# Kernel tuning notes

Hardware: AMD Instinct MI355X
Metric: run time of the kernel (lower is better)

Reference implementation:

```python
import jax, jax.numpy as jnp
import numpy as np

B, D, H, C = 8192, 384, 256, 6
K_MIN, K_MAX = 4, 16
LN_EPS = 1e-5


def setup_inputs() -> dict:
    key = jax.random.key(0)
    ks = jax.random.split(key, 6)
    s = lambda k, shape: (jax.random.normal(k, shape, jnp.float32) * 0.05)
    return {
        "x": jax.random.normal(ks[0], (B, D), jnp.float32),
        "W_proj": s(ks[1], (D, H)), "b_proj": jnp.zeros((H,), jnp.float32),
        "W_tau": s(ks[2], (D, 1)), "b_tau": jnp.zeros((1,), jnp.float32),
        "W_res": s(ks[3], (H, H)), "b_res": jnp.zeros((H,), jnp.float32),
        "ln_g": jnp.ones((H,), jnp.float32), "ln_b": jnp.zeros((H,), jnp.float32),
        "W_fc": s(ks[4], (H, C)), "b_fc": jnp.zeros((C,), jnp.float32),
    }


def reference(x, W_proj, b_proj, W_tau, b_tau, W_res, b_res, ln_g, ln_b, W_fc, b_fc):
    # adaptive k per sample (torch path casts to int -> non-differentiable)
    tau = jax.nn.sigmoid(x @ W_tau + b_tau)[:, 0]                      # [B]
    k = jax.lax.stop_gradient(
        jnp.clip(jnp.round(K_MAX - (K_MAX - K_MIN) * tau), 1, K_MAX)
    ).astype(jnp.int32)                                                # [B]

    # pairwise squared distances (same nearest-neighbor ordering as cdist)
    sq = jnp.sum(x * x, axis=-1)                                       # [B]
    d2 = sq[:, None] + sq[None, :] - 2.0 * (x @ x.T)                   # [B,B]
    _, idx = jax.lax.top_k(-jax.lax.stop_gradient(d2), K_MAX)          # [B,K_MAX] nearest (incl. self)

    h = jax.nn.relu(x @ W_proj + b_proj)                               # [B,H]

    # ragged top-k mean via fixed K_MAX gather + position mask
    gathered = h[idx]                                                  # [B,K_MAX,H]
    mask = (jnp.arange(K_MAX)[None, :] < k[:, None]).astype(h.dtype)   # [B,K_MAX]
    agg = jnp.einsum('bkh,bk->bh', gathered, mask) / k[:, None].astype(h.dtype)

    r = jax.nn.relu(agg @ W_res + b_res)                               # [B,H]
    z = h + r
    mu = jnp.mean(z, axis=-1, keepdims=True)
    var = jnp.var(z, axis=-1, keepdims=True)
    zn = (z - mu) / jnp.sqrt(var + LN_EPS)
    return (zn * ln_g + ln_b) @ W_fc + b_fc                            # [B,C]
```

## Files before the change

### kernel.cpp

```cpp
#include <hip/hip_runtime.h>
#include <hip/hip_fp16.h>
#include <math.h>

#define NROWS 8192
#define DDIM 384
#define HDIM 256
#define CDIM 6
#define LN_EPS 1e-5f
#define DSTR 138

typedef short bf16x8 __attribute__((ext_vector_type(8)));
typedef float f32x4 __attribute__((ext_vector_type(4)));
typedef unsigned short u16x8 __attribute__((ext_vector_type(8)));
typedef unsigned short u16x4 __attribute__((ext_vector_type(4)));
typedef unsigned short u16x2 __attribute__((ext_vector_type(2)));

__device__ __forceinline__ bool dj_better(float d1, int j1, float d2, int j2) {
    return (d1 < d2) || (d1 == d2 && j1 < j2);
}

__device__ __forceinline__ unsigned int umin_(unsigned int a, unsigned int b) { return a < b ? a : b; }
__device__ __forceinline__ unsigned int umax_(unsigned int a, unsigned int b) { return a > b ? a : b; }

__device__ __forceinline__ unsigned short map16f(float v) {
    union { _Float16 f; unsigned short u; } c;
    c.f = (_Float16)v;
    unsigned short b = c.u;
    return (unsigned short)(b ^ (unsigned short)((((short)b) >> 15) | 0x8000));
}

__device__ __forceinline__ float unmap16(unsigned int m16b) {
    unsigned short fb = (m16b & 0x8000u) ? (unsigned short)(m16b ^ 0x8000u)
                                         : (unsigned short)(~m16b);
    union { unsigned short u; _Float16 f; } cv; cv.u = fb;
    return (float)cv.f;
}

__device__ __forceinline__ unsigned short rne_bf16(float v) {
    unsigned int u = __float_as_uint(v);
    u += 0x7fffu + ((u >> 16) & 1u);
    return (unsigned short)(u >> 16);
}

__device__ __forceinline__ void ins8(
    unsigned int& s0, unsigned int& s1, unsigned int& s2, unsigned int& s3,
    unsigned int& s4, unsigned int& s5, unsigned int& s6, unsigned int& s7,
    unsigned int& m, unsigned int key)
{
    if (key < m) {
        s0 = (s0 == m) ? key : s0;
        s1 = (s1 == m) ? key : s1;
        s2 = (s2 == m) ? key : s2;
        s3 = (s3 == m) ? key : s3;
        s4 = (s4 == m) ? key : s4;
        s5 = (s5 == m) ? key : s5;
        s6 = (s6 == m) ? key : s6;
        s7 = (s7 == m) ? key : s7;
        m = umax_(umax_(umax_(s0, s1), umax_(s2, s3)),
                  umax_(umax_(s4, s5), umax_(s6, s7)));
    }
}

__device__ __forceinline__ unsigned int max8_(
    unsigned int s0, unsigned int s1, unsigned int s2, unsigned int s3,
    unsigned int s4, unsigned int s5, unsigned int s6, unsigned int s7)
{
    return umax_(umax_(umax_(s0, s1), umax_(s2, s3)),
                 umax_(umax_(s4, s5), umax_(s6, s7)));
}

__device__ __forceinline__ void sins8(
    unsigned int& s0, unsigned int& s1, unsigned int& s2, unsigned int& s3,
    unsigned int& s4, unsigned int& s5, unsigned int& s6, unsigned int& s7,
    unsigned int key)
{
    unsigned int t = umin_(s0, key);
    s0 = umax_(t, s1); t = umin_(t, s1);
    s1 = umax_(t, s2); t = umin_(t, s2);
    s2 = umax_(t, s3); t = umin_(t, s3);
    s3 = umax_(t, s4); t = umin_(t, s4);
    s4 = umax_(t, s5); t = umin_(t, s5);
    s5 = umax_(t, s6); t = umin_(t, s6);
    s6 = umax_(t, s7); s7 = umin_(t, s7);
}

#define CE_(a, b) { unsigned int hi_ = umax_(a, b), lo_ = umin_(a, b); a = hi_; b = lo_; }
#define SORT8_DESC(s0, s1, s2, s3, s4, s5, s6, s7) \
    CE_(s0, s1) CE_(s2, s3) CE_(s4, s5) CE_(s6, s7) \
    CE_(s0, s2) CE_(s1, s3) CE_(s4, s6) CE_(s5, s7) \
    CE_(s1, s2) CE_(s5, s6) CE_(s0, s4) CE_(s3, s7) \
    CE_(s1, s5) CE_(s2, s6) \
    CE_(s1, s4) CE_(s3, s6) \
    CE_(s2, s4) CE_(s3, s5) \
    CE_(s3, s4)

__global__ void __launch_bounds__(256) prep_kernel(
    const float* __restrict__ x, const float* __restrict__ W_tau,
    const float* __restrict__ b_tau, unsigned short* __restrict__ xb,
    float* __restrict__ sq, int* __restrict__ kk,
    const float* __restrict__ Wp, unsigned short* __restrict__ wpT,
    const float* __restrict__ Wr, unsigned short* __restrict__ wrT)
{
    int tid = threadIdx.x;
    if (blockIdx.x < NROWS / 4) {
        int wave = tid >> 6, lane = tid & 63;
        int row = blockIdx.x * 4 + wave;
        const float* xr = x + (size_t)row * DDIM;
        unsigned short* xbr = xb + (size_t)row * DDIM;
        float s = 0.f, tp = 0.f;
        #pragma unroll
        for (int q = 0; q < 6; ++q) {
            float v = xr[lane + 64 * q];
            xbr[lane + 64 * q] = rne_bf16(v);
            s = fmaf(v, v, s);
            tp = fmaf(v, W_tau[lane + 64 * q], tp);
        }
        #pragma unroll
        for (int off = 32; off > 0; off >>= 1) {
            s += __shfl_xor(s, off);
            tp += __shfl_xor(tp, off);
        }
        if (lane == 0) {
            sq[row] = s;
            float u = tp + b_tau[0];
            float tau = 1.f / (1.f + expf(-u));
            float kf = rintf(16.f - 12.f * tau);
            int k = (int)kf;
            k = min(16, max(1, k));
            kk[row] = k;
        }
    } else {
        int i = (blockIdx.x - NROWS / 4) * 256 + tid;
        if (i < DDIM * HDIM) {
            int k = i / HDIM, n = i % HDIM;
            wpT[(size_t)n * DDIM + k] = rne_bf16(Wp[i]);
        } else {
            int j = i - DDIM * HDIM;
            if (j < HDIM * HDIM) {
                int k = j / HDIM, n = j % HDIM;
                wrT[(size_t)n * HDIM + k] = rne_bf16(Wr[j]);
            }
        }
    }
}

__global__ void __launch_bounds__(256) mfma_gemm_bias_relu_kernel(
    const unsigned short* __restrict__ A, const unsigned short* __restrict__ WT,
    const float* __restrict__ bias, float* __restrict__ out,
    unsigned short* __restrict__ hb, int K)
{
    __shared__ unsigned short Abuf[128 * 32];
    __shared__ unsigned short Bbuf[128 * 32];

    const int tid = threadIdx.x;
    const int wave = tid >> 6;
    const int rowbase = blockIdx.x * 128;
    const int nbase = blockIdx.y * 128;
    const int lane = tid & 63;
    const int wr = (wave >> 1) * 64;
    const int wc = (wave & 1) * 64;
    const int m16 = lane & 15;
    const int kq = lane >> 4;

    const int er0 = tid >> 2;
    const int er1 = 64 + (tid >> 2);
    const int eko = tid & 3;

    f32x4 acc[4][4];
    #pragma unroll
    for (int a = 0; a < 4; ++a)
        #pragma unroll
        for (int b = 0; b < 4; ++b)
            acc[a][b] = (f32x4){0.f, 0.f, 0.f, 0.f};

    for (int kb = 0; kb < K / 32; ++kb) {
        const int k0 = kb * 32;
        __syncthreads();
        __builtin_amdgcn_global_load_lds(
            (const __attribute__((address_space(1))) void*)(A + (size_t)(rowbase + er0) * K + k0 + eko * 8),
            (__attribute__((address_space(3))) void*)((char*)Abuf + (wave * 64) * 16), 16, 0, 0);
        __builtin_amdgcn_global_load_lds(
            (const __attribute__((address_space(1))) void*)(A + (size_t)(rowbase + er1) * K + k0 + eko * 8),
            (__attribute__((address_space(3))) void*)((char*)Abuf + (256 + wave * 64) * 16), 16, 0, 0);
        __builtin_amdgcn_global_load_lds(
            (const __attribute__((address_space(1))) void*)(WT + (size_t)(nbase + er0) * K + k0 + eko * 8),
            (__attribute__((address_space(3))) void*)((char*)Bbuf + (wave * 64) * 16), 16, 0, 0);
        __builtin_amdgcn_global_load_lds(
            (const __attribute__((address_space(1))) void*)(WT + (size_t)(nbase + er1) * K + k0 + eko * 8),
            (__attribute__((address_space(3))) void*)((char*)Bbuf + (256 + wave * 64) * 16), 16, 0, 0);
        __syncthreads();

        bf16x8 af[4], bfr[4];
        #pragma unroll
        for (int s = 0; s < 4; ++s) {
            af[s]  = *(const bf16x8*)&Abuf[(wr + s * 16 + m16) * 32 + kq * 8];
            bfr[s] = *(const bf16x8*)&Bbuf[(wc + s * 16 + m16) * 32 + kq * 8];
        }
        #pragma unroll
        for (int si = 0; si < 4; ++si)
            #pragma unroll
            for (int sj = 0; sj < 4; ++sj)
                acc[si][sj] = __builtin_amdgcn_mfma_f32_16x16x32_bf16(
                    af[si], bfr[sj], acc[si][sj], 0, 0, 0);
    }

    #pragma unroll
    for (int sj = 0; sj < 4; ++sj) {
        int c = nbase + wc + sj * 16 + m16;
        float bc = bias[c];
        #pragma unroll
        for (int si = 0; si < 4; ++si) {
            int r = rowbase + wr + si * 16 + kq * 4;
            #pragma unroll
            for (int v = 0; v < 4; ++v) {
                float val = fmaxf(acc[si][sj][v] + bc, 0.f);
                out[(size_t)(r + v) * HDIM + c] = val;
                if (hb) hb[(size_t)(r + v) * HDIM + c] = rne_bf16(val);
            }
        }
    }
}

__global__ void __launch_bounds__(256) dist_topk_kernel(
    const unsigned short* __restrict__ xb, const float* __restrict__ sq,
    unsigned int* __restrict__ keys)
{
    __shared__ __align__(16) unsigned short SMEM[128 * DSTR];
    unsigned short* Abuf = SMEM;
    unsigned short* Bbuf = SMEM + 128 * 32;
    unsigned short* Dt   = SMEM;

    int t = blockIdx.x;
    int bi = (int)((sqrtf(8.f * (float)t + 1.f) - 1.f) * 0.5f);
    while ((bi + 1) * (bi + 2) / 2 <= t) ++bi;
    while (bi * (bi + 1) / 2 > t) --bi;
    int bj = t - bi * (bi + 1) / 2;

    const int tid = threadIdx.x;
    const int wave = tid >> 6;
    const int lane = tid & 63;
    const int rowbase = bi * 128;
    const int colbase = bj * 128;
    const int wr = (wave >> 1) * 64;
    const int wc = (wave & 1) * 64;
    const int m16 = lane & 15;
    const int kq = lane >> 4;

    const int er0 = tid >> 2;
    const int er1 = 64 + (tid >> 2);
    const int eko = tid & 3;

    f32x4 acc[4][4];
    #pragma unroll
    for (int a = 0; a < 4; ++a)
        #pragma unroll
        for (int b = 0; b < 4; ++b)
            acc[a][b] = (f32x4){0.f, 0.f, 0.f, 0.f};

    for (int kb = 0; kb < DDIM / 32; ++kb) {
        const int k0 = kb * 32;
        __syncthreads();
        __builtin_amdgcn_global_load_lds(
            (const __attribute__((address_space(1))) void*)(xb + (size_t)(rowbase + er0) * DDIM + k0 + eko * 8),
            (__attribute__((address_space(3))) void*)((char*)Abuf + (wave * 64) * 16), 16, 0, 0);
        __builtin_amdgcn_global_load_lds(
            (const __attribute__((address_space(1))) void*)(xb + (size_t)(rowbase + er1) * DDIM + k0 + eko * 8),
            (__attribute__((address_space(3))) void*)((char*)Abuf + (256 + wave * 64) * 16), 16, 0, 0);
        __builtin_amdgcn_global_load_lds(
            (const __attribute__((address_space(1))) void*)(xb + (size_t)(colbase + er0) * DDIM + k0 + eko * 8),
            (__attribute__((address_space(3))) void*)((char*)Bbuf + (wave * 64) * 16), 16, 0, 0);
        __builtin_amdgcn_global_load_lds(
            (const __attribute__((address_space(1))) void*)(xb + (size_t)(colbase + er1) * DDIM + k0 + eko * 8),
            (__attribute__((address_space(3))) void*)((char*)Bbuf + (256 + wave * 64) * 16), 16, 0, 0);
        __syncthreads();

        bf16x8 af[4], bfr[4];
        #pragma unroll
        for (int s = 0; s < 4; ++s) {
            af[s]  = *(const bf16x8*)&Abuf[(wr + s * 16 + m16) * 32 + kq * 8];
            bfr[s] = *(const bf16x8*)&Bbuf[(wc + s * 16 + m16) * 32 + kq * 8];
        }
        #pragma unroll
        for (int si = 0; si < 4; ++si)
            #pragma unroll
            for (int sj = 0; sj < 4; ++sj)
                acc[si][sj] = __builtin_amdgcn_mfma_f32_16x16x32_bf16(
                    af[si], bfr[sj], acc[si][sj], 0, 0, 0);
    }
    __syncthreads();

    const int sr = tid >> 1;
    const int seg = tid & 1;

    {
        float sqc[4];
        #pragma unroll
        for (int sj = 0; sj < 4; ++sj) sqc[sj] = sq[colbase + wc + sj * 16 + m16];
        #pragma unroll
        for (int si = 0; si < 4; ++si)
            #pragma unroll
            for (int sj = 0; sj < 4; ++sj) {
                int r = wr + si * 16 + kq * 4;
                int c = wc + sj * 16 + m16;
                #pragma unroll
                for (int v = 0; v < 4; ++v)
                    Dt[(r + v) * DSTR + c] = map16f(sqc[sj] - 2.0f * acc[si][sj][v]);
            }
        __syncthreads();

        const unsigned short* rowp = &Dt[sr * DSTR + seg * 64];
        const int cb0 = colbase + seg * 64;
        u16x8 c0 = *(const u16x8*)rowp;
        unsigned int s0 = ((unsigned int)c0[0] << 13) | (unsigned int)(cb0 + 0);
        unsigned int s1 = ((unsigned int)c0[1] << 13) | (unsigned int)(cb0 + 1);
        unsigned int s2 = ((unsigned int)c0[2] << 13) | (unsigned int)(cb0 + 2);
        unsigned int s3 = ((unsigned int)c0[3] << 13) | (unsigned int)(cb0 + 3);
        unsigned int s4 = ((unsigned int)c0[4] << 13) | (unsigned int)(cb0 + 4);
        unsigned int s5 = ((unsigned int)c0[5] << 13) | (unsigned int)(cb0 + 5);
        unsigned int s6 = ((unsigned int)c0[6] << 13) | (unsigned int)(cb0 + 6);
        unsigned int s7 = ((unsigned int)c0[7] << 13) | (unsigned int)(cb0 + 7);
        SORT8_DESC(s0, s1, s2, s3, s4, s5, s6, s7);
        #pragma unroll
        for (int i = 1; i < 8; ++i) {
            u16x8 ch = *(const u16x8*)(rowp + i * 8);
            int cb = cb0 + i * 8;
            #pragma unroll
            for (int e = 0; e < 8; ++e)
                sins8(s0, s1, s2, s3, s4, s5, s6, s7,
                      ((unsigned int)ch[e] << 13) | (unsigned int)(cb + e));
        }
        size_t kb = (size_t)(rowbase + sr) * 1024 + (size_t)bj * 16 + seg * 8;
        uint4 o0; o0.x = s0; o0.y = s1; o0.z = s2; o0.w = s3;
        uint4 o1; o1.x = s4; o1.y = s5; o1.z = s6; o1.w = s7;
        *(uint4*)&keys[kb] = o0;
        *(uint4*)&keys[kb + 4] = o1;
    }

    if (bi != bj) {
        __syncthreads();
        #pragma unroll
        for (int si = 0; si < 4; ++si) {
            float4 sqr4 = *(const float4*)&sq[rowbase + wr + si * 16 + kq * 4];
            float srw[4] = {sqr4.x, sqr4.y, sqr4.z, sqr4.w};
            #pragma unroll
            for (int sj = 0; sj < 4; ++sj) {
                int r = wr + si * 16 + kq * 4;
                int c = wc + sj * 16 + m16;
                unsigned short h4[4];
                #pragma unroll
                for (int v = 0; v < 4; ++v)
                    h4[v] = map16f(srw[v] - 2.0f * acc[si][sj][v]);
                *(unsigned long long*)&Dt[c * DSTR + r] = *(unsigned long long*)h4;
            }
        }
        __syncthreads();

        const unsigned short* rowp = &Dt[sr * DSTR + seg * 64];
        const int cb0 = rowbase + seg * 64;
        u16x8 c0 = *(const u16x8*)rowp;
        unsigned int s0 = ((unsigned int)c0[0] << 13) | (unsigned int)(cb0 + 0);
        unsigned int s1 = ((unsigned int)c0[1] << 13) | (unsigned int)(cb0 + 1);
        unsigned int s2 = ((unsigned int)c0[2] << 13) | (unsigned int)(cb0 + 2);
        unsigned int s3 = ((unsigned int)c0[3] << 13) | (unsigned int)(cb0 + 3);
        unsigned int s4 = ((unsigned int)c0[4] << 13) | (unsigned int)(cb0 + 4);
        unsigned int s5 = ((unsigned int)c0[5] << 13) | (unsigned int)(cb0 + 5);
        unsigned int s6 = ((unsigned int)c0[6] << 13) | (unsigned int)(cb0 + 6);
        unsigned int s7 = ((unsigned int)c0[7] << 13) | (unsigned int)(cb0 + 7);
        SORT8_DESC(s0, s1, s2, s3, s4, s5, s6, s7);
        #pragma unroll
        for (int i = 1; i < 8; ++i) {
            u16x8 ch = *(const u16x8*)(rowp + i * 8);
            int cb = cb0 + i * 8;
            #pragma unroll
            for (int e = 0; e < 8; ++e)
                sins8(s0, s1, s2, s3, s4, s5, s6, s7,
                      ((unsigned int)ch[e] << 13) | (unsigned int)(cb + e));
        }
        size_t kb = (size_t)(colbase + sr) * 1024 + (size_t)bi * 16 + seg * 8;
        uint4 o0; o0.x = s0; o0.y = s1; o0.z = s2; o0.w = s3;
        uint4 o1; o1.x = s4; o1.y = s5; o1.z = s6; o1.w = s7;
        *(uint4*)&keys[kb] = o0;
        *(uint4*)&keys[kb + 4] = o1;
    }
}

__global__ void __launch_bounds__(256) topk_rescore_agg_kernel(
    const unsigned int* __restrict__ keys, const float* __restrict__ x,
    const float* __restrict__ sq, const int* __restrict__ kk,
    const unsigned short* __restrict__ hb, unsigned short* __restrict__ aggb)
{
    const int w = threadIdx.x >> 6;
    const int row = blockIdx.x * 4 + w;
    const int lane = threadIdx.x & 63;
    __shared__ int sidx[4][16];

    const uint4* kp = (const uint4*)(keys + (size_t)row * 1024 + lane * 16);
    uint4 v0 = kp[0], v1 = kp[1];
    unsigned int s0 = v0.x, s1 = v0.y, s2 = v0.z, s3 = v0.w;
    unsigned int s4 = v1.x, s5 = v1.y, s6 = v1.z, s7 = v1.w;
    unsigned int m = max8_(s0, s1, s2, s3, s4, s5, s6, s7);
    #pragma unroll
    for (int q = 2; q < 4; ++q) {
        uint4 v = kp[q];
        unsigned int gmin = umin_(umin_(v.x, v.y), umin_(v.z, v.w));
        if (gmin < m) {
            ins8(s0, s1, s2, s3, s4, s5, s6, s7, m, v.x);
            ins8(s0, s1, s2, s3, s4, s5, s6, s7, m, v.y);
            ins8(s0, s1, s2, s3, s4, s5, s6, s7, m, v.z);
            ins8(s0, s1, s2, s3, s4, s5, s6, s7, m, v.w);
        }
    }
    unsigned int lmin = umin_(umin_(umin_(s0, s1), umin_(s2, s3)),
                              umin_(umin_(s4, s5), umin_(s6, s7)));
    unsigned int myout = 0;
    for (int t = 0; t < 32; ++t) {
        unsigned int wv = lmin;
        #pragma unroll
        for (int off = 32; off > 0; off >>= 1)
            wv = umin_(wv, (unsigned int)__shfl_xor((int)wv, off));
        if (lane == t) myout = wv;
        if (lmin == wv) {
            s0 = (s0 == wv) ? 0xFFFFFFFFu : s0;
            s1 = (s1 == wv) ? 0xFFFFFFFFu : s1;
            s2 = (s2 == wv) ? 0xFFFFFFFFu : s2;
            s3 = (s3 == wv) ? 0xFFFFFFFFu : s3;
            s4 = (s4 == wv) ? 0xFFFFFFFFu : s4;
            s5 = (s5 == wv) ? 0xFFFFFFFFu : s5;
            s6 = (s6 == wv) ? 0xFFFFFFFFu : s6;
            s7 = (s7 == wv) ? 0xFFFFFFFFu : s7;
            lmin = umin_(umin_(umin_(s0, s1), umin_(s2, s3)),
                         umin_(umin_(s4, s5), umin_(s6, s7)));
        }
    }
    int myj = (int)(myout & 8191u);
    float dscr = (lane < 32) ? unmap16(myout >> 13) : INFINITY;

    const float EPS2 = 2.5f;
    const int k = kk[row];
    float d_k   = __shfl(dscr, k);
    float d_km1 = __shfl(dscr, k - 1);
    bool cin = false, amb = false;
    if (lane < 32) {
        if (lane < k) { cin = (dscr + EPS2 <= d_k); amb = !cin; }
        else          { amb = (dscr < d_km1 + EPS2); }
    }
    unsigned long long cinmask = __ballot(cin);
    unsigned long long ambmask = __ballot(amb);
    int n_in = __popcll(cinmask);
    int msel = k - n_in;

    float d_ex = 0.f;
    if (msel > 0) {
        float xr[6];
        #pragma unroll
        for (int q = 0; q < 6; ++q) xr[q] = x[(size_t)row * DDIM + lane + 64 * q];
        float sqrow = sq[row];
        unsigned long long mm = ambmask;
        while (mm) {
            int c = (int)(__ffsll(mm) - 1);
            mm &= mm - 1;
            int j = __shfl(myj, c);
            const float* xc = x + (size_t)j * DDIM;
            float p = 0.f;
            #pragma unroll
            for (int q = 0; q < 6; ++q) p = fmaf(xr[q], xc[lane + 64 * q], p);
            #pragma unroll
            for (int off = 32; off > 0; off >>= 1) p += __shfl_xor(p, off);
            float d = sqrow + sq[j] - 2.f * p;
            if (lane == c) d_ex = d;
        }
        int selrank = 0;
        unsigned long long mm2 = ambmask;
        while (mm2) {
            int u = (int)(__ffsll(mm2) - 1);
            mm2 &= mm2 - 1;
            float du = __shfl(d_ex, u);
            int ju = __shfl(myj, u);
            if (u != lane && dj_better(du, ju, d_ex, myj)) ++selrank;
        }
        if (amb && selrank < msel)
            sidx[w][n_in + selrank] = myj;
    }
    if (cin) {
        int pos = __popcll(cinmask & ((1ull << lane) - 1ull));
        sidx[w][pos] = myj;
    }
    __syncthreads();

    float a0 = 0.f, a1 = 0.f, a2 = 0.f, a3 = 0.f;
    for (int t = 0; t < k; ++t) {
        uint2 v = *(const uint2*)(hb + (size_t)sidx[w][t] * HDIM + lane * 4);
        a0 += __uint_as_float(v.x << 16);
        a1 += __uint_as_float(v.x & 0xFFFF0000u);
        a2 += __uint_as_float(v.y << 16);
        a3 += __uint_as_float(v.y & 0xFFFF0000u);
    }
    float inv = 1.f / (float)k;
    unsigned int b0 = rne_bf16(a0 * inv);
    unsigned int b1 = rne_bf16(a1 * inv);
    unsigned int b2 = rne_bf16(a2 * inv);
    unsigned int b3 = rne_bf16(a3 * inv);
    uint2 o; o.x = b0 | (b1 << 16); o.y = b2 | (b3 << 16);
    *(uint2*)(aggb + (size_t)row * HDIM + lane * 4) = o;
}

__global__ void __launch_bounds__(256) ln_fc_kernel(
    const float* __restrict__ h, const float* __restrict__ r,
    const float* __restrict__ g, const float* __restrict__ bb,
    const float* __restrict__ W_fc, const float* __restrict__ b_fc,
    float* __restrict__ out)
{
    const int row = blockIdx.x * 4 + (threadIdx.x >> 6);
    const int lane = threadIdx.x & 63;
    const float* hp = h + (size_t)row * HDIM;
    const float* rp = r + (size_t)row * HDIM;

    float z[4];
    #pragma unroll
    for (int q = 0; q < 4; ++q)
        z[q] = hp[lane + 64 * q] + rp[lane + 64 * q];

    float s = z[0] + z[1] + z[2] + z[3];
    float s2 = z[0]*z[0] + z[1]*z[1] + z[2]*z[2] + z[3]*z[3];
    #pragma unroll
    for (int off = 32; off > 0; off >>= 1) {
        s += __shfl_xor(s, off);
        s2 += __shfl_xor(s2, off);
    }
    float mu = s / 256.f;
    float rstd = rsqrtf(s2 / 256.f - mu * mu + LN_EPS);

    float p[6] = {0.f, 0.f, 0.f, 0.f, 0.f, 0.f};
    #pragma unroll
    for (int q = 0; q < 4; ++q) {
        int i = lane + 64 * q;
        float val = (z[q] - mu) * rstd * g[i] + bb[i];
        #pragma unroll
        for (int c = 0; c < 6; ++c)
            p[c] = fmaf(val, W_fc[i * 6 + c], p[c]);
    }
    #pragma unroll
    for (int c = 0; c < 6; ++c)
        #pragma unroll
        for (int off = 32; off > 0; off >>= 1) p[c] += __shfl_xor(p[c], off);

    if (lane < 6) {
        float o = p[0];
        o = (lane == 1) ? p[1] : o;
        o = (lane == 2) ? p[2] : o;
        o = (lane == 3) ? p[3] : o;
        o = (lane == 4) ? p[4] : o;
        o = (lane == 5) ? p[5] : o;
        out[(size_t)row * CDIM + lane] = o + b_fc[lane];
    }
}

extern "C" void kernel_launch(void* const* d_in, const int* in_sizes, int n_in,
                              void* d_out, int out_size, void* d_ws, size_t ws_size,
                              hipStream_t stream) {
    const float* x      = (const float*)d_in[0];
    const float* W_proj = (const float*)d_in[1];
    const float* b_proj = (const float*)d_in[2];
    const float* W_tau  = (const float*)d_in[3];
    const float* b_tau  = (const float*)d_in[4];
    const float* W_res  = (const float*)d_in[5];
    const float* b_res  = (const float*)d_in[6];
    const float* ln_g   = (const float*)d_in[7];
    const float* ln_b   = (const float*)d_in[8];
    const float* W_fc   = (const float*)d_in[9];
    const float* b_fc   = (const float*)d_in[10];
    float* out = (float*)d_out;

    char* ws = (char*)d_ws;
    float* sq   = (float*)ws;                        ws += (size_t)NROWS * 4;
    int*   kk   = (int*)ws;                          ws += (size_t)NROWS * 4;
    float* h    = (float*)ws;                        ws += (size_t)NROWS * HDIM * 4;
    float* r    = (float*)ws;                        ws += (size_t)NROWS * HDIM * 4;
    unsigned short* xb   = (unsigned short*)ws;      ws += (size_t)NROWS * DDIM * 2;
    unsigned short* hbuf = (unsigned short*)ws;      ws += (size_t)NROWS * HDIM * 2;
    unsigned short* aggb = (unsigned short*)ws;      ws += (size_t)NROWS * HDIM * 2;
    unsigned short* wpT  = (unsigned short*)ws;      ws += (size_t)DDIM * HDIM * 2;
    unsigned short* wrT  = (unsigned short*)ws;      ws += (size_t)HDIM * HDIM * 2;
    ws = (char*)(((size_t)ws + 255) & ~(size_t)255);
    unsigned int* keys = (unsigned int*)ws;          ws += (size_t)NROWS * 1024 * 4;

    const int prepW = (DDIM * HDIM + HDIM * HDIM + 255) / 256;
    prep_kernel<<<NROWS / 4 + prepW, 256, 0, stream>>>(
        x, W_tau, b_tau, xb, sq, kk, W_proj, wpT, W_res, wrT);
    mfma_gemm_bias_relu_kernel<<<dim3(NROWS / 128, HDIM / 128), 256, 0, stream>>>(
        xb, wpT, b_proj, h, hbuf, DDIM);
    dist_topk_kernel<<<(NROWS/128) * (NROWS/128 + 1) / 2, 256, 0, stream>>>(xb, sq, keys);
    topk_rescore_agg_kernel<<<NROWS / 4, 256, 0, stream>>>(keys, x, sq, kk, hbuf, aggb);
    mfma_gemm_bias_relu_kernel<<<dim3(NROWS / 128, HDIM / 128), 256, 0, stream>>>(
        aggb, wrT, b_res, r, (unsigned short*)nullptr, HDIM);
    ln_fc_kernel<<<NROWS / 4, 256, 0, stream>>>(h, r, ln_g, ln_b, W_fc, b_fc, out);
}
```

Before: 229.3 us.

## Double-buffer GEMM k-loop and fuse projection GEMM into distance kernel

Factors the MFMA k-loop into a shared helper that double-buffers LDS tiles, so the next slice's global-to-LDS load is issued before the current slice's MFMAs and only one barrier runs per iteration. The projection GEMM is merged into the distance/top-k launch as extra leading blocks, which removes a kernel launch and lets the small GEMM overlap with the distance tiles. LDS use in the standalone GEMM doubles to 32KB. The distance kernel reuses its 128*DSTR shared buffer, which is large enough for both buffer sets.

```diff
diff --git a/kernel.cpp b/kernel.cpp
--- a/kernel.cpp
+++ b/kernel.cpp
@@ -8,6 +8,8 @@
 #define CDIM 6
 #define LN_EPS 1e-5f
 #define DSTR 138
+#define NTILES ((NROWS/128) * (NROWS/128 + 1) / 2)
+#define NGEMM1 ((NROWS/128) * (HDIM/128))
 
 typedef short bf16x8 __attribute__((ext_vector_type(8)));
 typedef float f32x4 __attribute__((ext_vector_type(4)));
@@ -144,57 +146,53 @@
     }
 }
 
-__global__ void __launch_bounds__(256) mfma_gemm_bias_relu_kernel(
-    const unsigned short* __restrict__ A, const unsigned short* __restrict__ WT,
-    const float* __restrict__ bias, float* __restrict__ out,
-    unsigned short* __restrict__ hb, int K)
-{
-    __shared__ unsigned short Abuf[128 * 32];
-    __shared__ unsigned short Bbuf[128 * 32];
-
+__device__ __forceinline__ void gemm_kloop(
+    const unsigned short* __restrict__ A, const unsigned short* __restrict__ B,
+    const int K, const int rowbase, const int nbase,
+    unsigned short* S, f32x4 (&acc)[4][4])
+{
     const int tid = threadIdx.x;
     const int wave = tid >> 6;
-    const int rowbase = blockIdx.x * 128;
-    const int nbase = blockIdx.y * 128;
     const int lane = tid & 63;
     const int wr = (wave >> 1) * 64;
     const int wc = (wave & 1) * 64;
     const int m16 = lane & 15;
     const int kq = lane >> 4;
-
     const int er0 = tid >> 2;
     const int er1 = 64 + (tid >> 2);
     const int eko = tid & 3;
-
-    f32x4 acc[4][4];
-    #pragma unroll
-    for (int a = 0; a < 4; ++a)
-        #pragma unroll
-        for (int b = 0; b < 4; ++b)
-            acc[a][b] = (f32x4){0.f, 0.f, 0.f, 0.f};
-
-    for (int kb = 0; kb < K / 32; ++kb) {
+    const int NK = K >> 5;
+
+    auto stage = [&](int kb, int set) {
         const int k0 = kb * 32;
-        __syncthreads();
+        char* Ad = (char*)S + set * 8192;
+        char* Bd = (char*)S + 16384 + set * 8192;
         __builtin_amdgcn_global_load_lds(
             (const __attribute__((address_space(1))) void*)(A + (size_t)(rowbase + er0) * K + k0 + eko * 8),
-            (__attribute__((address_space(3))) void*)((char*)Abuf + (wave * 64) * 16), 16, 0, 0);
+            (__attribute__((address_space(3))) void*)(Ad + (wave * 64) * 16), 16, 0, 0);
         __builtin_amdgcn_global_load_lds(
             (const __attribute__((address_space(1))) void*)(A + (size_t)(rowbase + er1) * K + k0 + eko * 8),
-            (__attribute__((address_space(3))) void*)((char*)Abuf + (256 + wave * 64) * 16), 16, 0, 0);
+            (__attribute__((address_space(3))) void*)(Ad + (256 + wave * 64) * 16), 16, 0, 0);
         __builtin_amdgcn_global_load_lds(
-            (const __attribute__((address_space(1))) void*)(WT + (size_t)(nbase + er0) * K + k0 + eko * 8),
-            (__attribute__((address_space(3))) void*)((char*)Bbuf + (wave * 64) * 16), 16, 0, 0);
+            (const __attribute__((address_space(1))) void*)(B + (size_t)(nbase + er0) * K + k0 + eko * 8),
+            (__attribute__((address_space(3))) void*)(Bd + (wave * 64) * 16), 16, 0, 0);
         __builtin_amdgcn_global_load_lds(
-            (const __attribute__((address_space(1))) void*)(WT + (size_t)(nbase + er1) * K + k0 + eko * 8),
-            (__attribute__((address_space(3))) void*)((char*)Bbuf + (256 + wave * 64) * 16), 16, 0, 0);
-        __syncthreads();
-
+            (const __attribute__((address_space(1))) void*)(B + (size_t)(nbase + er1) * K + k0 + eko * 8),
+            (__attribute__((address_space(3))) void*)(Bd + (256 + wave * 64) * 16), 16, 0, 0);
+    };
+
+    stage(0, 0);
+    __syncthreads();
+    for (int kb = 0; kb < NK; ++kb) {
+        const int cur = kb & 1;
+        if (kb + 1 < NK) stage(kb + 1, cur ^ 1);
+        const unsigned short* Ab = S + cur * 4096;
+        const unsigned short* Bb = S + 8192 + cur * 4096;
         bf16x8 af[4], bfr[4];
         #pragma unroll
         for (int s = 0; s < 4; ++s) {
-            af[s]  = *(const bf16x8*)&Abuf[(wr + s * 16 + m16) * 32 + kq * 8];
-            bfr[s] = *(const bf16x8*)&Bbuf[(wc + s * 16 + m16) * 32 + kq * 8];
+            af[s]  = *(const bf16x8*)&Ab[(wr + s * 16 + m16) * 32 + kq * 8];
+            bfr[s] = *(const bf16x8*)&Bb[(wc + s * 16 + m16) * 32 + kq * 8];
         }
         #pragma unroll
         for (int si = 0; si < 4; ++si)
@@ -202,8 +200,21 @@
             for (int sj = 0; sj < 4; ++sj)
                 acc[si][sj] = __builtin_amdgcn_mfma_f32_16x16x32_bf16(
                     af[si], bfr[sj], acc[si][sj], 0, 0, 0);
-    }
-
+        __syncthreads();
+    }
+}
+
+__device__ __forceinline__ void gemm_epilogue(
+    const float* __restrict__ bias, float* __restrict__ out,
+    unsigned short* __restrict__ hb, const int rowbase, const int nbase,
+    f32x4 (&acc)[4][4])
+{
+    const int lane = threadIdx.x & 63;
+    const int wave = threadIdx.x >> 6;
+    const int wr = (wave >> 1) * 64;
+    const int wc = (wave & 1) * 64;
+    const int m16 = lane & 15;
+    const int kq = lane >> 4;
     #pragma unroll
     for (int sj = 0; sj < 4; ++sj) {
         int c = nbase + wc + sj * 16 + m16;
@@ -221,16 +232,46 @@
     }
 }
 
-__global__ void __launch_bounds__(256) dist_topk_kernel(
+__global__ void __launch_bounds__(256) mfma_gemm_bias_relu_kernel(
+    const unsigned short* __restrict__ A, const unsigned short* __restrict__ WT,
+    const float* __restrict__ bias, float* __restrict__ out,
+    unsigned short* __restrict__ hb, int K)
+{
+    __shared__ __align__(16) unsigned short S[16384];
+    f32x4 acc[4][4];
+    #pragma unroll
+    for (int a = 0; a < 4; ++a)
+        #pragma unroll
+        for (int b = 0; b < 4; ++b)
+            acc[a][b] = (f32x4){0.f, 0.f, 0.f, 0.f};
+    gemm_kloop(A, WT, K, blockIdx.x * 128, blockIdx.y * 128, S, acc);
+    gemm_epilogue(bias, out, hb, blockIdx.x * 128, blockIdx.y * 128, acc);
+}
+
+__global__ void __launch_bounds__(256) dist_gemm_fused_kernel(
     const unsigned short* __restrict__ xb, const float* __restrict__ sq,
-    unsigned int* __restrict__ keys)
+    unsigned int* __restrict__ keys,
+    const unsigned short* __restrict__ wpT, const float* __restrict__ b_proj,
+    float* __restrict__ h, unsigned short* __restrict__ hb)
 {
     __shared__ __align__(16) unsigned short SMEM[128 * DSTR];
-    unsigned short* Abuf = SMEM;
-    unsigned short* Bbuf = SMEM + 128 * 32;
-    unsigned short* Dt   = SMEM;
-
-    int t = blockIdx.x;
+
+    f32x4 acc[4][4];
+    #pragma unroll
+    for (int a = 0; a < 4; ++a)
+        #pragma unroll
+        for (int b = 0; b < 4; ++b)
+            acc[a][b] = (f32x4){0.f, 0.f, 0.f, 0.f};
+
+    if (blockIdx.x < NGEMM1) {
+        const int rb = (blockIdx.x >> 1) * 128;
+        const int nb = (blockIdx.x & 1) * 128;
+        gemm_kloop(xb, wpT, DDIM, rb, nb, SMEM, acc);
+        gemm_epilogue(b_proj, h, hb, rb, nb, acc);
+        return;
+    }
+
+    int t = blockIdx.x - NGEMM1;
     int bi = (int)((sqrtf(8.f * (float)t + 1.f) - 1.f) * 0.5f);
     while ((bi + 1) * (bi + 2) / 2 <= t) ++bi;
     while (bi * (bi + 1) / 2 > t) --bi;
@@ -246,48 +287,8 @@
     const int m16 = lane & 15;
     const int kq = lane >> 4;
 
-    const int er0 = tid >> 2;
-    const int er1 = 64 + (tid >> 2);
-    const int eko = tid & 3;
-
-    f32x4 acc[4][4];
-    #pragma unroll
-    for (int a = 0; a < 4; ++a)
-        #pragma unroll
-        for (int b = 0; b < 4; ++b)
-            acc[a][b] = (f32x4){0.f, 0.f, 0.f, 0.f};
-
-    for (int kb = 0; kb < DDIM / 32; ++kb) {
-        const int k0 = kb * 32;
-        __syncthreads();
-        __builtin_amdgcn_global_load_lds(
-            (const __attribute__((address_space(1))) void*)(xb + (size_t)(rowbase + er0) * DDIM + k0 + eko * 8),
-            (__attribute__((address_space(3))) void*)((char*)Abuf + (wave * 64) * 16), 16, 0, 0);
-        __builtin_amdgcn_global_load_lds(
-            (const __attribute__((address_space(1))) void*)(xb + (size_t)(rowbase + er1) * DDIM + k0 + eko * 8),
-            (__attribute__((address_space(3))) void*)((char*)Abuf + (256 + wave * 64) * 16), 16, 0, 0);
-        __builtin_amdgcn_global_load_lds(
-            (const __attribute__((address_space(1))) void*)(xb + (size_t)(colbase + er0) * DDIM + k0 + eko * 8),
-            (__attribute__((address_space(3))) void*)((char*)Bbuf + (wave * 64) * 16), 16, 0, 0);
-        __builtin_amdgcn_global_load_lds(
-            (const __attribute__((address_space(1))) void*)(xb + (size_t)(colbase + er1) * DDIM + k0 + eko * 8),
-            (__attribute__((address_space(3))) void*)((char*)Bbuf + (256 + wave * 64) * 16), 16, 0, 0);
-        __syncthreads();
-
-        bf16x8 af[4], bfr[4];
-        #pragma unroll
-        for (int s = 0; s < 4; ++s) {
-            af[s]  = *(const bf16x8*)&Abuf[(wr + s * 16 + m16) * 32 + kq * 8];
-            bfr[s] = *(const bf16x8*)&Bbuf[(wc + s * 16 + m16) * 32 + kq * 8];
-        }
-        #pragma unroll
-        for (int si = 0; si < 4; ++si)
-            #pragma unroll
-            for (int sj = 0; sj < 4; ++sj)
-                acc[si][sj] = __builtin_amdgcn_mfma_f32_16x16x32_bf16(
-                    af[si], bfr[sj], acc[si][sj], 0, 0, 0);
-    }
-    __syncthreads();
+    gemm_kloop(xb, xb, DDIM, rowbase, colbase, SMEM, acc);
+    unsigned short* Dt = SMEM;
 
     const int sr = tid >> 1;
     const int seg = tid & 1;
@@ -587,9 +588,8 @@
     const int prepW = (DDIM * HDIM + HDIM * HDIM + 255) / 256;
     prep_kernel<<<NROWS / 4 + prepW, 256, 0, stream>>>(
         x, W_tau, b_tau, xb, sq, kk, W_proj, wpT, W_res, wrT);
-    mfma_gemm_bias_relu_kernel<<<dim3(NROWS / 128, HDIM / 128), 256, 0, stream>>>(
-        xb, wpT, b_proj, h, hbuf, DDIM);
-    dist_topk_kernel<<<(NROWS/128) * (NROWS/128 + 1) / 2, 256, 0, stream>>>(xb, sq, keys);
+    dist_gemm_fused_kernel<<<NGEMM1 + NTILES, 256, 0, stream>>>(
+        xb, sq, keys, wpT, b_proj, h, hbuf);
     topk_rescore_agg_kernel<<<NROWS / 4, 256, 0, stream>>>(keys, x, sq, kk, hbuf, aggb);
     mfma_gemm_bias_relu_kernel<<<dim3(NROWS / 128, HDIM / 128), 256, 0, stream>>>(
         aggb, wrT, b_res, r, (unsigned short*)nullptr, HDIM);
```

After: 219.3 us. 4.4% less time.
